# Kernel tuning notes

Hardware: AMD Instinct MI355X
Metric: run time of the kernel (lower is better)

## Reference

```python
import jax, jax.numpy as jnp
import numpy as np

B, S, IN, OUT, H, L, NH, STEPS = 256, 128, 64, 64, 1024, 2, 4, 16
HD = H // NH


def setup_inputs() -> dict:
    key = jax.random.key(0)
    ks = iter(jax.random.split(key, 32))
    std_h = 1.0 / np.sqrt(H)

    def u(k, shape, std):
        return jax.random.uniform(k, shape, jnp.float32, -std, std)

    inp = {"x": jax.random.normal(next(ks), (B, S, IN), jnp.float32)}
    # LSTM cells: stacked gate weights, gate order (i, f, g, o); y = x@Wx + h@Wh + b
    for name, din in (("e0", IN), ("e1", H), ("d0", OUT), ("d1", H)):
        inp[name + "_Wx"] = u(next(ks), (din, 4 * H), std_h)
        inp[name + "_Wh"] = u(next(ks), (H, 4 * H), std_h)
        inp[name + "_b"] = u(next(ks), (4 * H,), std_h)
    # attention linears (x@W + b convention)
    for name in ("Wq", "Wk", "Wv", "Wo"):
        inp[name] = u(next(ks), (H, H), std_h)
    for name in ("bq", "bk", "bv", "bo"):
        inp[name] = u(next(ks), (H,), std_h)
    inp["fc_W"] = u(next(ks), (2 * H, H), 1.0 / np.sqrt(2 * H))
    inp["fc_b"] = u(next(ks), (H,), 1.0 / np.sqrt(2 * H))
    inp["out_W"] = u(next(ks), (H, OUT), std_h)
    inp["out_b"] = u(next(ks), (OUT,), std_h)
    return inp


def _cell(x_t, h, c, Wx, Wh, b):
    z = x_t @ Wx + h @ Wh + b  # [B, 4H]
    i, f, g, o = jnp.split(z, 4, axis=-1)
    c = jax.nn.sigmoid(f) * c + jax.nn.sigmoid(i) * jnp.tanh(g)
    h = jax.nn.sigmoid(o) * jnp.tanh(c)
    return h, c


def _lstm_seq(x, Wx, Wh, b):
    # x: [B, T, D] -> outputs [B, T, H], final (h, c)
    h0 = jnp.zeros((x.shape[0], H), x.dtype)
    def step(carry, xt):
        h, c = carry
        h, c = _cell(xt, h, c, Wx, Wh, b)
        return (h, c), h
    (h, c), ys = jax.lax.scan(step, (h0, h0), jnp.swapaxes(x, 0, 1))
    return jnp.swapaxes(ys, 0, 1), h, c


def reference(x, e0_Wx, e0_Wh, e0_b, e1_Wx, e1_Wh, e1_b,
              d0_Wx, d0_Wh, d0_b, d1_Wx, d1_Wh, d1_b,
              Wq, bq, Wk, bk, Wv, bv, Wo, bo, fc_W, fc_b, out_W, out_b):
    # encoder: 2-layer manual LSTM (dropout=0, eval)
    y0, h0, c0 = _lstm_seq(x, e0_Wx, e0_Wh, e0_b)
    enc_out, h1, c1 = _lstm_seq(y0, e1_Wx, e1_Wh, e1_b)

    # K/V projections of encoder outputs (constant across decoder steps)
    Kp = (enc_out @ Wk + bk).reshape(B, S, NH, HD)
    Vp = (enc_out @ Wv + bv).reshape(B, S, NH, HD)
    scale = float(HD) ** 0.5

    def dstep(carry, _):
        dh0, dc0, dh1, dc1, xin = carry
        dh0, dc0 = _cell(xin, dh0, dc0, d0_Wx, d0_Wh, d0_b)
        dh1, dc1 = _cell(dh0, dh1, dc1, d1_Wx, d1_Wh, d1_b)
        q = (dh1 @ Wq + bq).reshape(B, NH, HD)
        scores = jnp.einsum('bnd,bsnd->bns', q, Kp) / scale
        w = jax.nn.softmax(scores, axis=-1)
        ctx = jnp.einsum('bns,bsnd->bnd', w, Vp).reshape(B, H)
        attn = ctx @ Wo + bo
        comb = jax.nn.relu(jnp.concatenate([dh1, attn], axis=-1) @ fc_W + fc_b)
        out = comb @ out_W + out_b  # [B, OUT]
        return (dh0, dc0, dh1, dc1, out), out

    init = (h0, c0, h1, c1, jnp.zeros((B, OUT), x.dtype))
    _, preds = jax.lax.scan(dstep, init, None, length=STEPS)
    return jnp.swapaxes(preds, 0, 1)  # [B, STEPS, OUT]
```

## Files before the change

kernel.cpp:

```cpp
#include <hip/hip_runtime.h>
#include <math.h>

typedef _Float16 h8 __attribute__((ext_vector_type(8)));
typedef _Float16 h4 __attribute__((ext_vector_type(4)));
typedef float f16v __attribute__((ext_vector_type(16)));

#define HPS 262144
#define XPS 2097152
#define IPS 16384
#define BSTR 40
#define BUFE (128 * BSTR)

__device__ __forceinline__ float4 ld4(const float* p) { return *(const float4*)p; }
__device__ __forceinline__ float sigf(float x) { return 1.0f / (1.0f + expf(-x)); }
__device__ __forceinline__ float bf2f(unsigned short u) { return __uint_as_float(((unsigned)u) << 16); }
__device__ __forceinline__ float rdin(const void* p, size_t i, int bf) {
  return bf ? bf2f(((const unsigned short*)p)[i]) : ((const float*)p)[i];
}

__global__ void detect_dtype(const unsigned short* __restrict__ probe, int n, int* flag) {
  __shared__ int cnt;
  if (threadIdx.x == 0) cnt = 0;
  __syncthreads();
  int c = 0;
  for (int i = threadIdx.x; i < n; i += 256) {
    int e = (probe[i] >> 7) & 0xFF;
    if (e >= 100 && e <= 126) c++;
  }
  atomicAdd(&cnt, c);
  __syncthreads();
  if (threadIdx.x == 0) *flag = (cnt > (n * 3) / 4) ? 1 : 0;
}

__global__ void cvt_f32(const void* __restrict__ in, float* __restrict__ out, int n,
                        const int* __restrict__ flag) {
  int bf = *flag;
  int i = blockIdx.x * 256 + threadIdx.x;
  if (i < n) out[i] = rdin(in, i, bf);
}

__global__ void tsplit(const void* __restrict__ in, int N,
                       _Float16* __restrict__ outHi, _Float16* __restrict__ outLo,
                       int ldo, int kOff, int pOff, const int* __restrict__ flag) {
  __shared__ float tile[32][33];
  int bf = *flag;
  int kb = blockIdx.x * 32, nb = blockIdx.y * 32;
  for (int r = threadIdx.y; r < 32; r += 8)
    tile[threadIdx.x][r] = rdin(in, (size_t)(kb + r) * N + nb + threadIdx.x, bf);
  __syncthreads();
  for (int r = threadIdx.y; r < 32; r += 8) {
    float v = tile[r][threadIdx.x];
    _Float16 hi = (_Float16)v;
    _Float16 lo = (_Float16)(v - (float)hi);
    size_t o = (size_t)(pOff + nb + r) * ldo + kOff + kb + threadIdx.x;
    outHi[o] = hi; outLo[o] = lo;
  }
}

__global__ void f2h_kernel(const void* __restrict__ in, _Float16* __restrict__ out, int n,
                           const int* __restrict__ flag) {
  int bf = *flag;
  int i = blockIdx.x * 1024 + threadIdx.x * 4;
  if (i < n) {
    float vv[4];
#pragma unroll
    for (int k = 0; k < 4; ++k) vv[k] = rdin(in, i + k, bf);
    h4 hv, lv;
#pragma unroll
    for (int k = 0; k < 4; ++k) { hv[k] = (_Float16)vv[k]; lv[k] = (_Float16)(vv[k] - (float)hv[k]); }
    *(h4*)(out + i) = hv;
    *(h4*)(out + n + i) = lv;
  }
}

__global__ void sentinel_kernel(float* out, float v) { out[0] = v; }

__device__ __forceinline__ void gemm_tile(
    const _Float16* __restrict__ A0, int lda0, int aps0,
    const _Float16* __restrict__ A1, int lda1, int aps1, int ksplit,
    const _Float16* __restrict__ WTh, const _Float16* __restrict__ WTl, int ldw,
    int pbase, int c0, int c1,
    float* __restrict__ zp, int zld, _Float16* Bs ) {
  const int tid = threadIdx.x;
  const int wv = tid >> 6, lane = tid & 63;
  const int l31 = lane & 31, lhi = lane >> 5;

  f16v acc00 = {}, acc01 = {}, acc10 = {}, acc11 = {};

  const int r0 = wv * 64 + l31;
  const int r1 = r0 + 32;
  const _Float16* a0b0 = A0 + (size_t)r0 * lda0;
  const _Float16* a1b0 = A1 + (size_t)r0 * lda1;
  const _Float16* a0b1 = A0 + (size_t)r1 * lda0;
  const _Float16* a1b1 = A1 + (size_t)r1 * lda1;

  const int spl = tid >> 7;
  const int sidx = tid & 127;
  const int sp = sidx >> 1;
  const int skh = (sidx & 1) << 4;
  const _Float16* srow = (spl ? WTl : WTh) + (size_t)(pbase + sp) * ldw + skh;
  const int sdoff = (spl * 64 + sp) * BSTR + skh;

  {
    const _Float16* s = srow + (c0 << 5);
    float4 v0 = *(const float4*)(s);
    float4 v1 = *(const float4*)(s + 8);
    _Float16* d = Bs + sdoff;
    *(float4*)(d) = v0;
    *(float4*)(d + 8) = v1;
  }

  int buf = 0;
  for (int c = c0; c < c1; ++c) {
    __syncthreads();
    float4 n0, n1;
    const bool more = (c + 1 < c1);
    if (more) {
      const _Float16* s = srow + ((c + 1) << 5);
      n0 = *(const float4*)(s);
      n1 = *(const float4*)(s + 8);
    }
    const _Float16* bb = Bs + buf * BUFE;
    int k0 = c << 5;
#pragma unroll
    for (int sub = 0; sub < 2; ++sub) {
      int ks = k0 + sub * 16 + lhi * 8;
      const _Float16 *pa0, *pa1; int ap;
      if (ks < ksplit) { pa0 = a0b0 + ks; pa1 = a0b1 + ks; ap = aps0; }
      else { int kk = ks - ksplit; pa0 = a1b0 + kk; pa1 = a1b1 + kk; ap = aps1; }
      h8 af0h = *(const h8*)pa0;
      h8 af0l = *(const h8*)(pa0 + ap);
      h8 af1h = *(const h8*)pa1;
      h8 af1l = *(const h8*)(pa1 + ap);
      int kl = sub * 16 + lhi * 8;
      h8 b0h = *(const h8*)(bb + (size_t)(l31) * BSTR + kl);
      h8 b0l = *(const h8*)(bb + (size_t)(64 + l31) * BSTR + kl);
      h8 b1h = *(const h8*)(bb + (size_t)(32 + l31) * BSTR + kl);
      h8 b1l = *(const h8*)(bb + (size_t)(96 + l31) * BSTR + kl);
      acc00 = __builtin_amdgcn_mfma_f32_32x32x16_f16(af0h, b0h, acc00, 0, 0, 0);
      acc00 = __builtin_amdgcn_mfma_f32_32x32x16_f16(af0h, b0l, acc00, 0, 0, 0);
      acc00 = __builtin_amdgcn_mfma_f32_32x32x16_f16(af0l, b0h, acc00, 0, 0, 0);
      acc01 = __builtin_amdgcn_mfma_f32_32x32x16_f16(af0h, b1h, acc01, 0, 0, 0);
      acc01 = __builtin_amdgcn_mfma_f32_32x32x16_f16(af0h, b1l, acc01, 0, 0, 0);
      acc01 = __builtin_amdgcn_mfma_f32_32x32x16_f16(af0l, b1h, acc01, 0, 0, 0);
      acc10 = __builtin_amdgcn_mfma_f32_32x32x16_f16(af1h, b0h, acc10, 0, 0, 0);
      acc10 = __builtin_amdgcn_mfma_f32_32x32x16_f16(af1h, b0l, acc10, 0, 0, 0);
      acc10 = __builtin_amdgcn_mfma_f32_32x32x16_f16(af1l, b0h, acc10, 0, 0, 0);
      acc11 = __builtin_amdgcn_mfma_f32_32x32x16_f16(af1h, b1h, acc11, 0, 0, 0);
      acc11 = __builtin_amdgcn_mfma_f32_32x32x16_f16(af1h, b1l, acc11, 0, 0, 0);
      acc11 = __builtin_amdgcn_mfma_f32_32x32x16_f16(af1l, b1h, acc11, 0, 0, 0);
    }
    if (more) {
      _Float16* d = Bs + (buf ^ 1) * BUFE + sdoff;
      *(float4*)(d) = n0;
      *(float4*)(d + 8) = n1;
    }
    buf ^= 1;
  }

#pragma unroll
  for (int mi = 0; mi < 2; ++mi) {
#pragma unroll
    for (int ni = 0; ni < 2; ++ni) {
      f16v av = (mi == 0) ? (ni == 0 ? acc00 : acc01) : (ni == 0 ? acc10 : acc11);
      int col = pbase + ni * 32 + l31;
#pragma unroll
      for (int r = 0; r < 16; ++r) {
        int row = wv * 64 + mi * 32 + (r & 3) + ((r >> 2) * 8) + lhi * 4;
        zp[(size_t)row * zld + col] = av[r];
      }
    }
  }
}

__global__ __launch_bounds__(256, 2) void enc_gemm(int t, int l1kq,
    const _Float16* xh, const _Float16* h0, const _Float16* h1,
    const _Float16* wt0h, const _Float16* wt0l,
    const _Float16* wt1h, const _Float16* wt1l,
    const _Float16* wtkvh, const _Float16* wtkvl,
    float* z0, float* z1, float* kvz) {
  __shared__ _Float16 Bs[2 * BUFE];
  int blk = blockIdx.x;
  int nl1 = 64 * l1kq;
  if (blk < nl1) {
    if (t < 1 || t > 128) return;
    int pg = blk & 63, kq = blk >> 6;
    int c0 = (64 * kq) / l1kq, c1 = (64 * (kq + 1)) / l1kq;
    gemm_tile(h0, 1024, HPS, h1, 1024, HPS, 1024, wt1h, wt1l, 2048,
              pg * 64, c0, c1, z1 + (size_t)kq * 1048576, 4096, Bs);
  } else if (blk < nl1 + 128) {
    if (t > 127) return;
    int w = blk - nl1, pg = w & 63, kq = w >> 6;
    gemm_tile(xh + (size_t)t * 64, 8192, XPS, h0, 1024, HPS, 64, wt0h, wt0l, 1088,
              pg * 64, kq * 17, kq * 17 + 17, z0 + (size_t)kq * 1048576, 4096, Bs);
  } else {
    if (t < 2) return;
    int w = blk - nl1 - 128, pg = w & 31, kq = w >> 5;
    gemm_tile(h1, 1024, HPS, h1, 1024, HPS, 1024, wtkvh, wtkvl, 1024,
              pg * 64, kq * 16, kq * 16 + 16, kvz + (size_t)kq * 524288, 2048, Bs);
  }
}

__global__ __launch_bounds__(256, 2) void gemm_k(
    const _Float16* A0, int lda0, int aps0,
    const _Float16* A1, int lda1, int aps1, int ksplit,
    const _Float16* WTh, const _Float16* WTl, int ldw,
    int npg, int nkq, int tot, int kqoff, float* zp, int zld) {
  __shared__ _Float16 Bs[2 * BUFE];
  int pg = blockIdx.x % npg, kq = blockIdx.x / npg + kqoff;
  int c0 = (tot * kq) / nkq, c1 = (tot * (kq + 1)) / nkq;
  gemm_tile(A0, lda0, aps0, A1, lda1, aps1, ksplit, WTh, WTl, ldw,
            pg * 64, c0, c1, zp + (size_t)kq * 256 * zld, zld, Bs);
}

__global__ __launch_bounds__(256, 2) void qfc_kernel(
    const _Float16* h1,
    const _Float16* wqh, const _Float16* wql,
    const _Float16* wfh, const _Float16* wfl,
    float* qp, float* fcp) {
  __shared__ _Float16 Bs[2 * BUFE];
  int blk = blockIdx.x;
  if (blk < 64) {
    int pg = blk & 15, kq = blk >> 4;
    gemm_tile(h1, 1024, HPS, h1, 1024, HPS, 1024, wqh, wql, 1024,
              pg * 64, kq * 8, kq * 8 + 8, qp + (size_t)kq * 262144, 1024, Bs);
  } else {
    int w = blk - 64, pg = w & 15, kq = w >> 4;
    gemm_tile(h1, 1024, HPS, h1, 1024, HPS, 1024, wfh, wfl, 2048,
              pg * 64, kq * 8, kq * 8 + 8, fcp + (size_t)kq * 262144, 1024, Bs);
  }
}

__device__ __forceinline__ void gates_body(const float* __restrict__ zp, int nparts,
    const float* __restrict__ bias, float* __restrict__ c,
    _Float16* __restrict__ h, int blk) {
  int e = blk * 1024 + threadIdx.x * 4;
  int b = e >> 10, j = e & 1023;
  size_t zrow = (size_t)b * 4096;
  float4 vi = ld4(bias + j), vf = ld4(bias + 1024 + j), vg = ld4(bias + 2048 + j), vo = ld4(bias + 3072 + j);
  for (int q = 0; q < nparts; ++q) {
    const float* zq = zp + (size_t)q * 1048576 + zrow;
    float4 t;
    t = ld4(zq + j);        vi.x += t.x; vi.y += t.y; vi.z += t.z; vi.w += t.w;
    t = ld4(zq + 1024 + j); vf.x += t.x; vf.y += t.y; vf.z += t.z; vf.w += t.w;
    t = ld4(zq + 2048 + j); vg.x += t.x; vg.y += t.y; vg.z += t.z; vg.w += t.w;
    t = ld4(zq + 3072 + j); vo.x += t.x; vo.y += t.y; vo.z += t.z; vo.w += t.w;
  }
  float* cp = c + (size_t)b * 1024 + j;
  float4 cv = ld4(cp);
  float zi[4] = {vi.x, vi.y, vi.z, vi.w}, zf[4] = {vf.x, vf.y, vf.z, vf.w};
  float zg[4] = {vg.x, vg.y, vg.z, vg.w}, zo[4] = {vo.x, vo.y, vo.z, vo.w};
  float cc[4] = {cv.x, cv.y, cv.z, cv.w};
  float hn[4];
#pragma unroll
  for (int k = 0; k < 4; ++k) {
    float ii = sigf(zi[k]), ff = sigf(zf[k]), gg = tanhf(zg[k]), oo = sigf(zo[k]);
    float cn = ff * cc[k] + ii * gg;
    cc[k] = cn;
    hn[k] = oo * tanhf(cn);
  }
  float4 co; co.x = cc[0]; co.y = cc[1]; co.z = cc[2]; co.w = cc[3];
  *(float4*)cp = co;
  h4 hv, lv;
#pragma unroll
  for (int k = 0; k < 4; ++k) { hv[k] = (_Float16)hn[k]; lv[k] = (_Float16)(hn[k] - (float)hv[k]); }
  *(h4*)(h + (size_t)b * 1024 + j) = hv;
  *(h4*)(h + HPS + (size_t)b * 1024 + j) = lv;
}

__global__ void enc_gates(int t, int l1parts, const float* z0, const float* z1, const float* kvz,
                          const float* b0, const float* b1,
                          const float* bk, const float* bv,
                          float* c0, float* c1, _Float16* h0, _Float16* h1,
                          _Float16* Kp, _Float16* Vp) {
  int blk = blockIdx.x;
  if (blk < 256) {
    if (t > 127) return;
    gates_body(z0, 2, b0, c0, h0, blk);
  } else if (blk < 512) {
    if (t < 1 || t > 128) return;
    gates_body(z1, l1parts, b1, c1, h1, blk - 256);
  } else {
    if (t < 2) return;
    int e = (blk - 512) * 1024 + threadIdx.x * 4;
    int b = e >> 11, col = e & 2047;
    const float* bb = (col < 1024) ? (bk + col) : (bv + col - 1024);
    float4 v = ld4(bb);
    for (int q = 0; q < 2; ++q) {
      float4 tt = ld4(kvz + (size_t)q * 524288 + e);
      v.x += tt.x; v.y += tt.y; v.z += tt.z; v.w += tt.w;
    }
    _Float16* dst = (col < 1024) ? Kp : Vp;
    int cc = (col < 1024) ? col : col - 1024;
    h4 hv; hv[0] = (_Float16)v.x; hv[1] = (_Float16)v.y; hv[2] = (_Float16)v.z; hv[3] = (_Float16)v.w;
    *(h4*)(dst + (size_t)(b * 128 + (t - 2)) * 1024 + cc) = hv;
  }
}

__global__ void dec_gates(const float* zp, int nparts, const float* bias,
                          float* c, _Float16* h) {
  gates_body(zp, nparts, bias, c, h, blockIdx.x);
}

__global__ void reduce_act(const float* __restrict__ zp, int nparts,
                           const float* __restrict__ bias, _Float16* __restrict__ out, int relu) {
  int e = blockIdx.x * 1024 + threadIdx.x * 4;
  int j = e & 1023;
  float4 v = ld4(bias + j);
  for (int q = 0; q < nparts; ++q) {
    float4 t = ld4(zp + (size_t)q * 262144 + e);
    v.x += t.x; v.y += t.y; v.z += t.z; v.w += t.w;
  }
  if (relu) {
    v.x = fmaxf(v.x, 0.f); v.y = fmaxf(v.y, 0.f); v.z = fmaxf(v.z, 0.f); v.w = fmaxf(v.w, 0.f);
  }
  float vv[4] = {v.x, v.y, v.z, v.w};
  h4 hv, lv;
#pragma unroll
  for (int k = 0; k < 4; ++k) { hv[k] = (_Float16)vv[k]; lv[k] = (_Float16)(vv[k] - (float)hv[k]); }
  *(h4*)(out + e) = hv;
  *(h4*)(out + HPS + e) = lv;
}

__global__ void out_reduce(const float* __restrict__ op, const float* __restrict__ outb,
                           float* __restrict__ dout, _Float16* __restrict__ xin, int s) {
  int e = blockIdx.x * 1024 + threadIdx.x * 4;
  int b = e >> 6, o = e & 63;
  float4 v = ld4(outb + o);
  for (int q = 0; q < 16; ++q) {
    float4 t = ld4(op + (size_t)q * 16384 + e);
    v.x += t.x; v.y += t.y; v.z += t.z; v.w += t.w;
  }
  *(float4*)(dout + (size_t)(b * 16 + s) * 64 + o) = v;
  float vv[4] = {v.x, v.y, v.z, v.w};
  h4 hv, lv;
#pragma unroll
  for (int k = 0; k < 4; ++k) { hv[k] = (_Float16)vv[k]; lv[k] = (_Float16)(vv[k] - (float)hv[k]); }
  *(h4*)(xin + e) = hv;
  *(h4*)(xin + IPS + e) = lv;
}

__global__ void attn_kernel(const float* __restrict__ qp, const float* __restrict__ bq,
                            const _Float16* __restrict__ Kp, const _Float16* __restrict__ Vp,
                            _Float16* __restrict__ ctx) {
  int b = blockIdx.x >> 2, n = blockIdx.x & 3;
  __shared__ float qs[256];
  __shared__ float sw[128];
  int tid = threadIdx.x;
  float qv = bq[n * 256 + tid];
  for (int q = 0; q < 4; ++q) qv += qp[(size_t)q * 262144 + (size_t)b * 1024 + n * 256 + tid];
  qs[tid] = qv;
  __syncthreads();
  int w = tid >> 6, lane = tid & 63;
  for (int s = w; s < 128; s += 4) {
    const _Float16* kr = Kp + (size_t)(b * 128 + s) * 1024 + n * 256;
    float acc = 0.f;
#pragma unroll
    for (int d = 0; d < 4; ++d) acc += qs[lane + d * 64] * (float)kr[lane + d * 64];
    for (int off = 32; off; off >>= 1) acc += __shfl_down(acc, off);
    if (lane == 0) sw[s] = acc * 0.0625f;
  }
  __syncthreads();
  if (w == 0) {
    float a = sw[lane], bb = sw[lane + 64];
    float m = fmaxf(a, bb);
    for (int off = 32; off; off >>= 1) m = fmaxf(m, __shfl_down(m, off));
    m = __shfl(m, 0);
    float e1 = expf(a - m), e2 = expf(bb - m);
    float ss = e1 + e2;
    for (int off = 32; off; off >>= 1) ss += __shfl_down(ss, off);
    ss = __shfl(ss, 0);
    float inv = 1.0f / ss;
    sw[lane] = e1 * inv; sw[lane + 64] = e2 * inv;
  }
  __syncthreads();
  float acc = 0.f;
  const _Float16* vb = Vp + (size_t)b * 131072 + n * 256 + tid;
  for (int s2 = 0; s2 < 128; ++s2) acc += sw[s2] * (float)vb[(size_t)s2 * 1024];
  size_t idx = (size_t)b * 1024 + n * 256 + tid;
  _Float16 hi = (_Float16)acc;
  ctx[idx] = hi;
  ctx[HPS + idx] = (_Float16)(acc - (float)hi);
}

extern "C" void kernel_launch(void* const* d_in, const int* in_sizes, int n_in,
                              void* d_out, int out_size, void* d_ws, size_t ws_size,
                              hipStream_t stream) {
  const void* x     = d_in[0];
  const void* e0_Wx = d_in[1];
  const void* e0_Wh = d_in[2];
  const void* e0_b  = d_in[3];
  const void* e1_Wx = d_in[4];
  const void* e1_Wh = d_in[5];
  const void* e1_b  = d_in[6];
  const void* d0_Wx = d_in[7];
  const void* d0_Wh = d_in[8];
  const void* d0_b  = d_in[9];
  const void* d1_Wx = d_in[10];
  const void* d1_Wh = d_in[11];
  const void* d1_b  = d_in[12];
  const void* Wq = d_in[13];
  const void* Wk = d_in[14];
  const void* Wv = d_in[15];
  const void* Wo = d_in[16];
  const void* bq = d_in[17];
  const void* bk = d_in[18];
  const void* bv = d_in[19];
  const void* bo = d_in[20];
  const void* fc_W  = d_in[21];
  const void* fc_b  = d_in[22];
  const void* out_W = d_in[23];
  const void* out_b = d_in[24];

  int l1parts = 4;
  char* p = (char*)d_ws;
  int* flag; float* bias_arena; char* warena; char* zero0;
  _Float16 *h0, *h1, *xin, *Kp, *Vp, *ctx, *attn_h, *comb;
  float *c0, *c1; float* zarena;
  size_t zeroBytes = 0;

  for (int attempt = 0; attempt < 2; ++attempt) {
    p = (char*)d_ws;
    auto alloc = [&](size_t bytes) { char* r = p; p += (bytes + 255) & ~(size_t)255; return r; };
    flag = (int*)alloc(256);
    bias_arena = (float*)alloc(87040);
    warena = alloc(68419584);
    zero0 = p;
    h0 = (_Float16*)alloc(1048576);
    h1 = (_Float16*)alloc(1048576);
    c0 = (float*)alloc(1048576);
    c1 = (float*)alloc(1048576);
    xin = (_Float16*)alloc(65536);
    zeroBytes = (size_t)(p - zero0);
    Kp = (_Float16*)alloc(67108864);
    Vp = (_Float16*)alloc(67108864);
    zarena = (float*)alloc((size_t)(3 + l1parts) * 4194304);
    ctx    = (_Float16*)alloc(1048576);
    attn_h = (_Float16*)alloc(1048576);
    comb   = (_Float16*)alloc(1048576);
    if ((size_t)(p - (char*)d_ws) <= ws_size) break;
    l1parts = 2;
  }
  if ((size_t)(p - (char*)d_ws) > ws_size) {
    sentinel_kernel<<<1, 1, 0, stream>>>((float*)d_out, 1.0e9f + (float)ws_size);
    return;
  }

  float* c_e0b = bias_arena +     0;
  float* c_e1b = bias_arena +  4096;
  float* c_d0b = bias_arena +  8192;
  float* c_d1b = bias_arena + 12288;
  float* c_bq  = bias_arena + 16384;
  float* c_bk  = bias_arena + 17408;
  float* c_bv  = bias_arena + 18432;
  float* c_bo  = bias_arena + 19456;
  float* c_fcb = bias_arena + 20480;
  float* c_ob  = bias_arena + 21504;

  _Float16* wt_e0h = (_Float16*)(warena);
  _Float16* wt_e0l = (_Float16*)(warena +  8912896);
  _Float16* wt_e1h = (_Float16*)(warena + 17825792);
  _Float16* wt_e1l = (_Float16*)(warena + 34603008);
  _Float16* wt_kvh = (_Float16*)(warena + 51380224);
  _Float16* wt_kvl = (_Float16*)(warena + 55574528);
  _Float16* xh     = (_Float16*)(warena + 59768832);
  _Float16* wt_d0h = (_Float16*)(warena);
  _Float16* wt_d0l = (_Float16*)(warena +  8912896);
  _Float16* wt_d1h = (_Float16*)(warena + 17825792);
  _Float16* wt_d1l = (_Float16*)(warena + 34603008);
  _Float16* wt_qh  = (_Float16*)(warena + 51380224);
  _Float16* wt_ql  = (_Float16*)(warena + 53477376);
  _Float16* wt_oh  = (_Float16*)(warena + 55574528);
  _Float16* wt_ol  = (_Float16*)(warena + 57671680);
  _Float16* wt_fch = (_Float16*)(warena + 59768832);
  _Float16* wt_fcl = (_Float16*)(warena + 63963136);
  _Float16* wt_outh= (_Float16*)(warena + 68157440);
  _Float16* wt_outl= (_Float16*)(warena + 68288512);

  float* z0e = zarena;
  float* z1e = zarena + 2097152;
  float* kvz = z1e + (size_t)l1parts * 1048576;
  float* zdec = zarena;
  float* fcp = zarena;
  float* qp  = zarena + 2097152;
  float* op  = zarena + 3145728;

  detect_dtype<<<1, 256, 0, stream>>>((const unsigned short*)e0_Wx, 16384, flag);
  cvt_f32<<<16, 256, 0, stream>>>(e0_b, c_e0b, 4096, flag);
  cvt_f32<<<16, 256, 0, stream>>>(e1_b, c_e1b, 4096, flag);
  cvt_f32<<<16, 256, 0, stream>>>(d0_b, c_d0b, 4096, flag);
  cvt_f32<<<16, 256, 0, stream>>>(d1_b, c_d1b, 4096, flag);
  cvt_f32<<<4, 256, 0, stream>>>(bq, c_bq, 1024, flag);
  cvt_f32<<<4, 256, 0, stream>>>(bk, c_bk, 1024, flag);
  cvt_f32<<<4, 256, 0, stream>>>(bv, c_bv, 1024, flag);
  cvt_f32<<<4, 256, 0, stream>>>(bo, c_bo, 1024, flag);
  cvt_f32<<<4, 256, 0, stream>>>(fc_b, c_fcb, 1024, flag);
  cvt_f32<<<1, 64, 0, stream>>>(out_b, c_ob, 64, flag);

  dim3 tb(32, 8);
  tsplit<<<dim3(2, 128), tb, 0, stream>>>(e0_Wx, 4096, wt_e0h, wt_e0l, 1088, 0, 0, flag);
  tsplit<<<dim3(32, 128), tb, 0, stream>>>(e0_Wh, 4096, wt_e0h, wt_e0l, 1088, 64, 0, flag);
  tsplit<<<dim3(32, 128), tb, 0, stream>>>(e1_Wx, 4096, wt_e1h, wt_e1l, 2048, 0, 0, flag);
  tsplit<<<dim3(32, 128), tb, 0, stream>>>(e1_Wh, 4096, wt_e1h, wt_e1l, 2048, 1024, 0, flag);
  tsplit<<<dim3(32, 32), tb, 0, stream>>>(Wk, 1024, wt_kvh, wt_kvl, 1024, 0, 0, flag);
  tsplit<<<dim3(32, 32), tb, 0, stream>>>(Wv, 1024, wt_kvh, wt_kvl, 1024, 0, 1024, flag);
  f2h_kernel<<<2048, 256, 0, stream>>>(x, xh, 2097152, flag);
  hipMemsetAsync(zero0, 0, zeroBytes, stream);

  int encBlocks = 64 * l1parts + 192;
  for (int t = 0; t <= 129; ++t) {
    enc_gemm<<<encBlocks, 256, 0, stream>>>(t, l1parts, xh, h0, h1,
                                            wt_e0h, wt_e0l, wt_e1h, wt_e1l,
                                            wt_kvh, wt_kvl, z0e, z1e, kvz);
    enc_gates<<<1024, 256, 0, stream>>>(t, l1parts, z0e, z1e, kvz, c_e0b, c_e1b, c_bk, c_bv,
                                        c0, c1, h0, h1, Kp, Vp);
  }

  tsplit<<<dim3(2, 128), tb, 0, stream>>>(d0_Wx, 4096, wt_d0h, wt_d0l, 1088, 0, 0, flag);
  tsplit<<<dim3(32, 128), tb, 0, stream>>>(d0_Wh, 4096, wt_d0h, wt_d0l, 1088, 64, 0, flag);
  tsplit<<<dim3(32, 128), tb, 0, stream>>>(d1_Wx, 4096, wt_d1h, wt_d1l, 2048, 0, 0, flag);
  tsplit<<<dim3(32, 128), tb, 0, stream>>>(d1_Wh, 4096, wt_d1h, wt_d1l, 2048, 1024, 0, flag);
  tsplit<<<dim3(32, 32), tb, 0, stream>>>(Wq, 1024, wt_qh, wt_ql, 1024, 0, 0, flag);
  tsplit<<<dim3(32, 32), tb, 0, stream>>>(Wo, 1024, wt_oh, wt_ol, 1024, 0, 0, flag);
  tsplit<<<dim3(64, 32), tb, 0, stream>>>(fc_W, 1024, wt_fch, wt_fcl, 2048, 0, 0, flag);
  tsplit<<<dim3(32, 2), tb, 0, stream>>>(out_W, 64, wt_outh, wt_outl, 1024, 0, 0, flag);

  for (int s = 0; s < 16; ++s) {
    gemm_k<<<256, 256, 0, stream>>>(xin, 64, IPS, h0, 1024, HPS, 64,
                                    wt_d0h, wt_d0l, 1088, 64, 4, 34, 0, zdec, 4096);
    dec_gates<<<256, 256, 0, stream>>>(zdec, 4, c_d0b, c0, h0);
    gemm_k<<<256, 256, 0, stream>>>(h0, 1024, HPS, h1, 1024, HPS, 1024,
                                    wt_d1h, wt_d1l, 2048, 64, 4, 64, 0, zdec, 4096);
    dec_gates<<<256, 256, 0, stream>>>(zdec, 4, c_d1b, c1, h1);
    qfc_kernel<<<128, 256, 0, stream>>>(h1, wt_qh, wt_ql, wt_fch, wt_fcl, qp, fcp);
    attn_kernel<<<1024, 256, 0, stream>>>(qp, c_bq, Kp, Vp, ctx);
    gemm_k<<<64, 256, 0, stream>>>(ctx, 1024, HPS, ctx, 1024, HPS, 1024,
                                   wt_oh, wt_ol, 1024, 16, 4, 32, 0, qp, 1024);
    reduce_act<<<256, 256, 0, stream>>>(qp, 4, c_bo, attn_h, 0);
    gemm_k<<<64, 256, 0, stream>>>(h1, 1024, HPS, attn_h, 1024, HPS, 1024,
                                   wt_fch, wt_fcl, 2048, 16, 8, 64, 4, fcp, 1024);
    reduce_act<<<256, 256, 0, stream>>>(fcp, 8, c_fcb, comb, 1);
    gemm_k<<<16, 256, 0, stream>>>(comb, 1024, HPS, comb, 1024, HPS, 1024,
                                   wt_outh, wt_outl, 1024, 1, 16, 32, 0, op, 64);
    out_reduce<<<16, 256, 0, stream>>>(op, c_ob, (float*)d_out, xin, s);
  }
}
```

Baseline: 9.562 ms.

## Fuse split-K reductions and gate activations into GEMM kernels via last-arrival counters

Removes the separate gate, reduce and output-reduction kernels. The last split-K block for each column group now sums the partials and applies the LSTM gates, bias, ReLU or output write, detected through an atomic arrival counter. Gate weight columns are interleaved (i,f,g,o per hidden unit) so one block's 64 columns cover 16 complete hidden units. h buffers are double-buffered to avoid read/write races once finishing happens inside the same launch. This roughly halves the number of kernel launches per recurrence step. In exchange it adds atomics and fences, and the finishing work runs serially in one block per column group.

```diff
diff --git a/kernel.cpp b/kernel.cpp
--- a/kernel.cpp
+++ b/kernel.cpp
@@ -11,6 +11,15 @@
 #define BSTR 40
 #define BUFE (128 * BSTR)
 
+#define COFF_L0 0
+#define COFF_L1 64
+#define COFF_KV 128
+#define COFF_D0 160
+#define COFF_D1 224
+#define COFF_WO 288
+#define COFF_FC 304
+#define COFF_OUT 320
+
 __device__ __forceinline__ float4 ld4(const float* p) { return *(const float4*)p; }
 __device__ __forceinline__ float sigf(float x) { return 1.0f / (1.0f + expf(-x)); }
 __device__ __forceinline__ float bf2f(unsigned short u) { return __uint_as_float(((unsigned)u) << 16); }
@@ -32,16 +41,19 @@
   if (threadIdx.x == 0) *flag = (cnt > (n * 3) / 4) ? 1 : 0;
 }
 
-__global__ void cvt_f32(const void* __restrict__ in, float* __restrict__ out, int n,
+__global__ void cvt_f32(const void* __restrict__ in, float* __restrict__ out, int n, int gp,
                         const int* __restrict__ flag) {
   int bf = *flag;
   int i = blockIdx.x * 256 + threadIdx.x;
-  if (i < n) out[i] = rdin(in, i, bf);
+  if (i < n) {
+    int o = gp ? (((i & 1023) << 2) | (i >> 10)) : i;
+    out[o] = rdin(in, i, bf);
+  }
 }
 
 __global__ void tsplit(const void* __restrict__ in, int N,
                        _Float16* __restrict__ outHi, _Float16* __restrict__ outLo,
-                       int ldo, int kOff, int pOff, const int* __restrict__ flag) {
+                       int ldo, int kOff, int pOff, int gp, const int* __restrict__ flag) {
   __shared__ float tile[32][33];
   int bf = *flag;
   int kb = blockIdx.x * 32, nb = blockIdx.y * 32;
@@ -52,7 +64,9 @@
     float v = tile[r][threadIdx.x];
     _Float16 hi = (_Float16)v;
     _Float16 lo = (_Float16)(v - (float)hi);
-    size_t o = (size_t)(pOff + nb + r) * ldo + kOff + kb + threadIdx.x;
+    int p = pOff + nb + r;
+    if (gp) p = ((p & 1023) << 2) | (p >> 10);
+    size_t o = (size_t)p * ldo + kOff + kb + threadIdx.x;
     outHi[o] = hi; outLo[o] = lo;
   }
 }
@@ -173,171 +187,265 @@
   }
 }
 
+__device__ __forceinline__ bool last_arrival(int* cnt, int nparts) {
+  __shared__ int sdone;
+  __syncthreads();
+  if (threadIdx.x == 0)
+    sdone = __hip_atomic_fetch_add(cnt, 1, __ATOMIC_ACQ_REL, __HIP_MEMORY_SCOPE_AGENT);
+  __syncthreads();
+  if (sdone == nparts - 1) {
+    if (threadIdx.x == 0)
+      __hip_atomic_store(cnt, 0, __ATOMIC_RELAXED, __HIP_MEMORY_SCOPE_AGENT);
+    __threadfence();
+    return true;
+  }
+  return false;
+}
+
+__device__ void lstm_finish(const float* __restrict__ z, size_t ps, int np, int zld,
+                            const float* __restrict__ pb, float* __restrict__ c,
+                            _Float16* __restrict__ h, int pg) {
+  int row = threadIdx.x;
+  const float* zr = z + (size_t)row * zld + pg * 64;
+  float* cr = c + (size_t)row * 1024 + pg * 16;
+  _Float16* hr = h + (size_t)row * 1024 + pg * 16;
+#pragma unroll
+  for (int half = 0; half < 2; ++half) {
+    float4 a[8];
+#pragma unroll
+    for (int u = 0; u < 8; ++u) a[u] = ld4(pb + pg * 64 + half * 32 + u * 4);
+    for (int q = 0; q < np; ++q) {
+      const float* zq = zr + (size_t)q * ps + half * 32;
+#pragma unroll
+      for (int u = 0; u < 8; ++u) {
+        float4 t = ld4(zq + u * 4);
+        a[u].x += t.x; a[u].y += t.y; a[u].z += t.z; a[u].w += t.w;
+      }
+    }
+    float4 cv0 = ld4(cr + half * 8), cv1 = ld4(cr + half * 8 + 4);
+    float cc[8] = {cv0.x, cv0.y, cv0.z, cv0.w, cv1.x, cv1.y, cv1.z, cv1.w};
+    h8 hh, hl;
+#pragma unroll
+    for (int u = 0; u < 8; ++u) {
+      float ii = sigf(a[u].x), ff = sigf(a[u].y), gg = tanhf(a[u].z), oo = sigf(a[u].w);
+      float cn = ff * cc[u] + ii * gg;
+      cc[u] = cn;
+      float hn = oo * tanhf(cn);
+      _Float16 hi = (_Float16)hn;
+      hh[u] = hi; hl[u] = (_Float16)(hn - (float)hi);
+    }
+    float4 co0 = {cc[0], cc[1], cc[2], cc[3]}, co1 = {cc[4], cc[5], cc[6], cc[7]};
+    *(float4*)(cr + half * 8) = co0;
+    *(float4*)(cr + half * 8 + 4) = co1;
+    *(h8*)(hr + half * 8) = hh;
+    *(h8*)(hr + HPS + half * 8) = hl;
+  }
+}
+
+__device__ void kv_finish(const float* __restrict__ z, size_t ps, int np, int zld,
+                          const float* __restrict__ bk, const float* __restrict__ bv,
+                          _Float16* __restrict__ Kp, _Float16* __restrict__ Vp, int pg, int t) {
+  int row = threadIdx.x;
+  int colb = pg * 64;
+  const float* zr = z + (size_t)row * zld + colb;
+  const float* bias = (colb < 1024) ? (bk + colb) : (bv + colb - 1024);
+  _Float16* dst = (colb < 1024) ? (Kp + (size_t)(row * 128 + (t - 2)) * 1024 + colb)
+                                : (Vp + (size_t)(row * 128 + (t - 2)) * 1024 + colb - 1024);
+#pragma unroll
+  for (int u = 0; u < 8; ++u) {
+    float4 a = ld4(bias + u * 8), b = ld4(bias + u * 8 + 4);
+    for (int q = 0; q < np; ++q) {
+      float4 t0 = ld4(zr + (size_t)q * ps + u * 8);
+      float4 t1 = ld4(zr + (size_t)q * ps + u * 8 + 4);
+      a.x += t0.x; a.y += t0.y; a.z += t0.z; a.w += t0.w;
+      b.x += t1.x; b.y += t1.y; b.z += t1.z; b.w += t1.w;
+    }
+    h8 hv;
+    hv[0] = (_Float16)a.x; hv[1] = (_Float16)a.y; hv[2] = (_Float16)a.z; hv[3] = (_Float16)a.w;
+    hv[4] = (_Float16)b.x; hv[5] = (_Float16)b.y; hv[6] = (_Float16)b.z; hv[7] = (_Float16)b.w;
+    *(h8*)(dst + u * 8) = hv;
+  }
+}
+
+__device__ void act_finish(const float* __restrict__ z, size_t ps, int np, int zld,
+                           const float* __restrict__ bias, _Float16* __restrict__ out,
+                           int relu, int pg) {
+  int row = threadIdx.x;
+  const float* zr = z + (size_t)row * zld + pg * 64;
+  _Float16* orow = out + (size_t)row * 1024 + pg * 64;
+#pragma unroll
+  for (int u = 0; u < 8; ++u) {
+    float4 a = ld4(bias + pg * 64 + u * 8), b = ld4(bias + pg * 64 + u * 8 + 4);
+    for (int q = 0; q < np; ++q) {
+      float4 t0 = ld4(zr + (size_t)q * ps + u * 8);
+      float4 t1 = ld4(zr + (size_t)q * ps + u * 8 + 4);
+      a.x += t0.x; a.y += t0.y; a.z += t0.z; a.w += t0.w;
+      b.x += t1.x; b.y += t1.y; b.z += t1.z; b.w += t1.w;
+    }
+    if (relu) {
+      a.x = fmaxf(a.x, 0.f); a.y = fmaxf(a.y, 0.f); a.z = fmaxf(a.z, 0.f); a.w = fmaxf(a.w, 0.f);
+      b.x = fmaxf(b.x, 0.f); b.y = fmaxf(b.y, 0.f); b.z = fmaxf(b.z, 0.f); b.w = fmaxf(b.w, 0.f);
+    }
+    float vv[8] = {a.x, a.y, a.z, a.w, b.x, b.y, b.z, b.w};
+    h8 hh, hl;
+#pragma unroll
+    for (int k = 0; k < 8; ++k) {
+      _Float16 hi = (_Float16)vv[k];
+      hh[k] = hi; hl[k] = (_Float16)(vv[k] - (float)hi);
+    }
+    *(h8*)(orow + u * 8) = hh;
+    *(h8*)(orow + HPS + u * 8) = hl;
+  }
+}
+
+__device__ void out_finish(const float* __restrict__ op, const float* __restrict__ ob,
+                           float* __restrict__ dout, _Float16* __restrict__ xin, int s) {
+  int row = threadIdx.x;
+  const float* zr = op + (size_t)row * 64;
+  float* dr = dout + (size_t)(row * 16 + s) * 64;
+#pragma unroll
+  for (int u = 0; u < 8; ++u) {
+    float4 a = ld4(ob + u * 8), b = ld4(ob + u * 8 + 4);
+    for (int q = 0; q < 16; ++q) {
+      float4 t0 = ld4(zr + (size_t)q * 16384 + u * 8);
+      float4 t1 = ld4(zr + (size_t)q * 16384 + u * 8 + 4);
+      a.x += t0.x; a.y += t0.y; a.z += t0.z; a.w += t0.w;
+      b.x += t1.x; b.y += t1.y; b.z += t1.z; b.w += t1.w;
+    }
+    *(float4*)(dr + u * 8) = a;
+    *(float4*)(dr + u * 8 + 4) = b;
+    float vv[8] = {a.x, a.y, a.z, a.w, b.x, b.y, b.z, b.w};
+    h8 hh, hl;
+#pragma unroll
+    for (int k = 0; k < 8; ++k) {
+      _Float16 hi = (_Float16)vv[k];
+      hh[k] = hi; hl[k] = (_Float16)(vv[k] - (float)hi);
+    }
+    *(h8*)(xin + row * 64 + u * 8) = hh;
+    *(h8*)(xin + IPS + row * 64 + u * 8) = hl;
+  }
+}
+
 __global__ __launch_bounds__(256, 2) void enc_gemm(int t, int l1kq,
-    const _Float16* xh, const _Float16* h0, const _Float16* h1,
+    const _Float16* xh, _Float16* h0a, _Float16* h0b, _Float16* h1a, _Float16* h1b,
     const _Float16* wt0h, const _Float16* wt0l,
     const _Float16* wt1h, const _Float16* wt1l,
     const _Float16* wtkvh, const _Float16* wtkvl,
-    float* z0, float* z1, float* kvz) {
+    float* z0, float* z1, float* kvz,
+    const float* pb0, const float* pb1, const float* bk, const float* bv,
+    float* c0, float* c1, _Float16* Kp, _Float16* Vp, int* cnts) {
   __shared__ _Float16 Bs[2 * BUFE];
   int blk = blockIdx.x;
   int nl1 = 64 * l1kq;
+  const int pr = (t - 1) & 1;
+  const _Float16* h0r = pr ? h0b : h0a;
+  const _Float16* h1r = pr ? h1b : h1a;
   if (blk < nl1) {
     if (t < 1 || t > 128) return;
     int pg = blk & 63, kq = blk >> 6;
-    int c0 = (64 * kq) / l1kq, c1 = (64 * (kq + 1)) / l1kq;
-    gemm_tile(h0, 1024, HPS, h1, 1024, HPS, 1024, wt1h, wt1l, 2048,
-              pg * 64, c0, c1, z1 + (size_t)kq * 1048576, 4096, Bs);
+    int cc0 = (64 * kq) / l1kq, cc1 = (64 * (kq + 1)) / l1kq;
+    gemm_tile(h0r, 1024, HPS, h1r, 1024, HPS, 1024, wt1h, wt1l, 2048,
+              pg * 64, cc0, cc1, z1 + (size_t)kq * 1048576, 4096, Bs);
+    if (last_arrival(cnts + COFF_L1 + pg, l1kq)) {
+      _Float16* h1w = (t & 1) ? h1b : h1a;
+      lstm_finish(z1, 1048576, l1kq, 4096, pb1, c1, h1w, pg);
+    }
   } else if (blk < nl1 + 128) {
     if (t > 127) return;
     int w = blk - nl1, pg = w & 63, kq = w >> 6;
-    gemm_tile(xh + (size_t)t * 64, 8192, XPS, h0, 1024, HPS, 64, wt0h, wt0l, 1088,
+    gemm_tile(xh + (size_t)t * 64, 8192, XPS, h0r, 1024, HPS, 64, wt0h, wt0l, 1088,
               pg * 64, kq * 17, kq * 17 + 17, z0 + (size_t)kq * 1048576, 4096, Bs);
+    if (last_arrival(cnts + COFF_L0 + pg, 2)) {
+      _Float16* h0w = (t & 1) ? h0b : h0a;
+      lstm_finish(z0, 1048576, 2, 4096, pb0, c0, h0w, pg);
+    }
   } else {
     if (t < 2) return;
     int w = blk - nl1 - 128, pg = w & 31, kq = w >> 5;
-    gemm_tile(h1, 1024, HPS, h1, 1024, HPS, 1024, wtkvh, wtkvl, 1024,
+    gemm_tile(h1r, 1024, HPS, h1r, 1024, HPS, 1024, wtkvh, wtkvl, 1024,
               pg * 64, kq * 16, kq * 16 + 16, kvz + (size_t)kq * 524288, 2048, Bs);
-  }
-}
-
-__global__ __launch_bounds__(256, 2) void gemm_k(
-    const _Float16* A0, int lda0, int aps0,
-    const _Float16* A1, int lda1, int aps1, int ksplit,
-    const _Float16* WTh, const _Float16* WTl, int ldw,
-    int npg, int nkq, int tot, int kqoff, float* zp, int zld) {
+    if (last_arrival(cnts + COFF_KV + pg, 2)) {
+      kv_finish(kvz, 524288, 2, 2048, bk, bv, Kp, Vp, pg, t);
+    }
+  }
+}
+
+__global__ __launch_bounds__(256, 2) void dec0_gemm(
+    const _Float16* xin, const _Float16* h0r,
+    const _Float16* wh, const _Float16* wl, const float* pb,
+    float* c0, _Float16* h0w, float* z, int* cnt) {
   __shared__ _Float16 Bs[2 * BUFE];
-  int pg = blockIdx.x % npg, kq = blockIdx.x / npg + kqoff;
-  int c0 = (tot * kq) / nkq, c1 = (tot * (kq + 1)) / nkq;
-  gemm_tile(A0, lda0, aps0, A1, lda1, aps1, ksplit, WTh, WTl, ldw,
-            pg * 64, c0, c1, zp + (size_t)kq * 256 * zld, zld, Bs);
+  int pg = blockIdx.x & 63, kq = blockIdx.x >> 6;
+  int cc0 = (34 * kq) / 4, cc1 = (34 * (kq + 1)) / 4;
+  gemm_tile(xin, 64, IPS, h0r, 1024, HPS, 64, wh, wl, 1088,
+            pg * 64, cc0, cc1, z + (size_t)kq * 1048576, 4096, Bs);
+  if (last_arrival(cnt + pg, 4))
+    lstm_finish(z, 1048576, 4, 4096, pb, c0, h0w, pg);
+}
+
+__global__ __launch_bounds__(256, 2) void dec1_gemm(
+    const _Float16* h0n, const _Float16* h1r,
+    const _Float16* wh, const _Float16* wl, const float* pb,
+    float* c1, _Float16* h1w, float* z, int* cnt) {
+  __shared__ _Float16 Bs[2 * BUFE];
+  int pg = blockIdx.x & 63, kq = blockIdx.x >> 6;
+  gemm_tile(h0n, 1024, HPS, h1r, 1024, HPS, 1024, wh, wl, 2048,
+            pg * 64, kq * 16, kq * 16 + 16, z + (size_t)kq * 1048576, 4096, Bs);
+  if (last_arrival(cnt + pg, 4))
+    lstm_finish(z, 1048576, 4, 4096, pb, c1, h1w, pg);
 }
 
 __global__ __launch_bounds__(256, 2) void qfc_kernel(
-    const _Float16* h1,
+    const _Float16* h1n,
     const _Float16* wqh, const _Float16* wql,
     const _Float16* wfh, const _Float16* wfl,
-    float* qp, float* fcp) {
+    float* qp, float* fcp, int* cnt_fc) {
   __shared__ _Float16 Bs[2 * BUFE];
   int blk = blockIdx.x;
   if (blk < 64) {
     int pg = blk & 15, kq = blk >> 4;
-    gemm_tile(h1, 1024, HPS, h1, 1024, HPS, 1024, wqh, wql, 1024,
+    gemm_tile(h1n, 1024, HPS, h1n, 1024, HPS, 1024, wqh, wql, 1024,
               pg * 64, kq * 8, kq * 8 + 8, qp + (size_t)kq * 262144, 1024, Bs);
   } else {
     int w = blk - 64, pg = w & 15, kq = w >> 4;
-    gemm_tile(h1, 1024, HPS, h1, 1024, HPS, 1024, wfh, wfl, 2048,
+    gemm_tile(h1n, 1024, HPS, h1n, 1024, HPS, 1024, wfh, wfl, 2048,
               pg * 64, kq * 8, kq * 8 + 8, fcp + (size_t)kq * 262144, 1024, Bs);
-  }
-}
-
-__device__ __forceinline__ void gates_body(const float* __restrict__ zp, int nparts,
-    const float* __restrict__ bias, float* __restrict__ c,
-    _Float16* __restrict__ h, int blk) {
-  int e = blk * 1024 + threadIdx.x * 4;
-  int b = e >> 10, j = e & 1023;
-  size_t zrow = (size_t)b * 4096;
-  float4 vi = ld4(bias + j), vf = ld4(bias + 1024 + j), vg = ld4(bias + 2048 + j), vo = ld4(bias + 3072 + j);
-  for (int q = 0; q < nparts; ++q) {
-    const float* zq = zp + (size_t)q * 1048576 + zrow;
-    float4 t;
-    t = ld4(zq + j);        vi.x += t.x; vi.y += t.y; vi.z += t.z; vi.w += t.w;
-    t = ld4(zq + 1024 + j); vf.x += t.x; vf.y += t.y; vf.z += t.z; vf.w += t.w;
-    t = ld4(zq + 2048 + j); vg.x += t.x; vg.y += t.y; vg.z += t.z; vg.w += t.w;
-    t = ld4(zq + 3072 + j); vo.x += t.x; vo.y += t.y; vo.z += t.z; vo.w += t.w;
-  }
-  float* cp = c + (size_t)b * 1024 + j;
-  float4 cv = ld4(cp);
-  float zi[4] = {vi.x, vi.y, vi.z, vi.w}, zf[4] = {vf.x, vf.y, vf.z, vf.w};
-  float zg[4] = {vg.x, vg.y, vg.z, vg.w}, zo[4] = {vo.x, vo.y, vo.z, vo.w};
-  float cc[4] = {cv.x, cv.y, cv.z, cv.w};
-  float hn[4];
-#pragma unroll
-  for (int k = 0; k < 4; ++k) {
-    float ii = sigf(zi[k]), ff = sigf(zf[k]), gg = tanhf(zg[k]), oo = sigf(zo[k]);
-    float cn = ff * cc[k] + ii * gg;
-    cc[k] = cn;
-    hn[k] = oo * tanhf(cn);
-  }
-  float4 co; co.x = cc[0]; co.y = cc[1]; co.z = cc[2]; co.w = cc[3];
-  *(float4*)cp = co;
-  h4 hv, lv;
-#pragma unroll
-  for (int k = 0; k < 4; ++k) { hv[k] = (_Float16)hn[k]; lv[k] = (_Float16)(hn[k] - (float)hv[k]); }
-  *(h4*)(h + (size_t)b * 1024 + j) = hv;
-  *(h4*)(h + HPS + (size_t)b * 1024 + j) = lv;
-}
-
-__global__ void enc_gates(int t, int l1parts, const float* z0, const float* z1, const float* kvz,
-                          const float* b0, const float* b1,
-                          const float* bk, const float* bv,
-                          float* c0, float* c1, _Float16* h0, _Float16* h1,
-                          _Float16* Kp, _Float16* Vp) {
-  int blk = blockIdx.x;
-  if (blk < 256) {
-    if (t > 127) return;
-    gates_body(z0, 2, b0, c0, h0, blk);
-  } else if (blk < 512) {
-    if (t < 1 || t > 128) return;
-    gates_body(z1, l1parts, b1, c1, h1, blk - 256);
-  } else {
-    if (t < 2) return;
-    int e = (blk - 512) * 1024 + threadIdx.x * 4;
-    int b = e >> 11, col = e & 2047;
-    const float* bb = (col < 1024) ? (bk + col) : (bv + col - 1024);
-    float4 v = ld4(bb);
-    for (int q = 0; q < 2; ++q) {
-      float4 tt = ld4(kvz + (size_t)q * 524288 + e);
-      v.x += tt.x; v.y += tt.y; v.z += tt.z; v.w += tt.w;
-    }
-    _Float16* dst = (col < 1024) ? Kp : Vp;
-    int cc = (col < 1024) ? col : col - 1024;
-    h4 hv; hv[0] = (_Float16)v.x; hv[1] = (_Float16)v.y; hv[2] = (_Float16)v.z; hv[3] = (_Float16)v.w;
-    *(h4*)(dst + (size_t)(b * 128 + (t - 2)) * 1024 + cc) = hv;
-  }
-}
-
-__global__ void dec_gates(const float* zp, int nparts, const float* bias,
-                          float* c, _Float16* h) {
-  gates_body(zp, nparts, bias, c, h, blockIdx.x);
-}
-
-__global__ void reduce_act(const float* __restrict__ zp, int nparts,
-                           const float* __restrict__ bias, _Float16* __restrict__ out, int relu) {
-  int e = blockIdx.x * 1024 + threadIdx.x * 4;
-  int j = e & 1023;
-  float4 v = ld4(bias + j);
-  for (int q = 0; q < nparts; ++q) {
-    float4 t = ld4(zp + (size_t)q * 262144 + e);
-    v.x += t.x; v.y += t.y; v.z += t.z; v.w += t.w;
-  }
-  if (relu) {
-    v.x = fmaxf(v.x, 0.f); v.y = fmaxf(v.y, 0.f); v.z = fmaxf(v.z, 0.f); v.w = fmaxf(v.w, 0.f);
-  }
-  float vv[4] = {v.x, v.y, v.z, v.w};
-  h4 hv, lv;
-#pragma unroll
-  for (int k = 0; k < 4; ++k) { hv[k] = (_Float16)vv[k]; lv[k] = (_Float16)(vv[k] - (float)hv[k]); }
-  *(h4*)(out + e) = hv;
-  *(h4*)(out + HPS + e) = lv;
-}
-
-__global__ void out_reduce(const float* __restrict__ op, const float* __restrict__ outb,
-                           float* __restrict__ dout, _Float16* __restrict__ xin, int s) {
-  int e = blockIdx.x * 1024 + threadIdx.x * 4;
-  int b = e >> 6, o = e & 63;
-  float4 v = ld4(outb + o);
-  for (int q = 0; q < 16; ++q) {
-    float4 t = ld4(op + (size_t)q * 16384 + e);
-    v.x += t.x; v.y += t.y; v.z += t.z; v.w += t.w;
-  }
-  *(float4*)(dout + (size_t)(b * 16 + s) * 64 + o) = v;
-  float vv[4] = {v.x, v.y, v.z, v.w};
-  h4 hv, lv;
-#pragma unroll
-  for (int k = 0; k < 4; ++k) { hv[k] = (_Float16)vv[k]; lv[k] = (_Float16)(vv[k] - (float)hv[k]); }
-  *(h4*)(xin + e) = hv;
-  *(h4*)(xin + IPS + e) = lv;
+    last_arrival(cnt_fc + pg, 8);
+  }
+}
+
+__global__ __launch_bounds__(256, 2) void wo_gemm(
+    const _Float16* ctx, const _Float16* wh, const _Float16* wl,
+    const float* bo, _Float16* attn_h, float* z, int* cnt) {
+  __shared__ _Float16 Bs[2 * BUFE];
+  int pg = blockIdx.x & 15, kq = blockIdx.x >> 4;
+  gemm_tile(ctx, 1024, HPS, ctx, 1024, HPS, 1024, wh, wl, 1024,
+            pg * 64, kq * 8, kq * 8 + 8, z + (size_t)kq * 262144, 1024, Bs);
+  if (last_arrival(cnt + pg, 4))
+    act_finish(z, 262144, 4, 1024, bo, attn_h, 0, pg);
+}
+
+__global__ __launch_bounds__(256, 2) void fc_gemm(
+    const _Float16* h1n, const _Float16* attn_h,
+    const _Float16* wh, const _Float16* wl,
+    const float* fcb, _Float16* comb, float* z, int* cnt) {
+  __shared__ _Float16 Bs[2 * BUFE];
+  int pg = blockIdx.x & 15, kq = (blockIdx.x >> 4) + 4;
+  gemm_tile(h1n, 1024, HPS, attn_h, 1024, HPS, 1024, wh, wl, 2048,
+            pg * 64, kq * 8, kq * 8 + 8, z + (size_t)kq * 262144, 1024, Bs);
+  if (last_arrival(cnt + pg, 8))
+    act_finish(z, 262144, 8, 1024, fcb, comb, 1, pg);
+}
+
+__global__ __launch_bounds__(256, 2) void out_gemm(
+    const _Float16* comb, const _Float16* wh, const _Float16* wl,
+    const float* ob, float* dout, _Float16* xin, float* z, int s, int* cnt) {
+  __shared__ _Float16 Bs[2 * BUFE];
+  int kq = blockIdx.x;
+  gemm_tile(comb, 1024, HPS, comb, 1024, HPS, 1024, wh, wl, 1024,
+            0, kq * 2, kq * 2 + 2, z + (size_t)kq * 16384, 64, Bs);
+  if (last_arrival(cnt, 16))
+    out_finish(z, ob, dout, xin, s);
 }
 
 __global__ void attn_kernel(const float* __restrict__ qp, const float* __restrict__ bq,
@@ -415,7 +523,8 @@
   int l1parts = 4;
   char* p = (char*)d_ws;
   int* flag; float* bias_arena; char* warena; char* zero0;
-  _Float16 *h0, *h1, *xin, *Kp, *Vp, *ctx, *attn_h, *comb;
+  int* cnts;
+  _Float16 *h0a, *h0b, *h1a, *h1b, *xin, *Kp, *Vp, *ctx, *attn_h, *comb;
   float *c0, *c1; float* zarena;
   size_t zeroBytes = 0;
 
@@ -426,8 +535,11 @@
     bias_arena = (float*)alloc(87040);
     warena = alloc(68419584);
     zero0 = p;
-    h0 = (_Float16*)alloc(1048576);
-    h1 = (_Float16*)alloc(1048576);
+    cnts = (int*)alloc(2048);
+    h0a = (_Float16*)alloc(1048576);
+    h0b = (_Float16*)alloc(1048576);
+    h1a = (_Float16*)alloc(1048576);
+    h1b = (_Float16*)alloc(1048576);
     c0 = (float*)alloc(1048576);
     c1 = (float*)alloc(1048576);
     xin = (_Float16*)alloc(65536);
@@ -486,62 +598,61 @@
   float* op  = zarena + 3145728;
 
   detect_dtype<<<1, 256, 0, stream>>>((const unsigned short*)e0_Wx, 16384, flag);
-  cvt_f32<<<16, 256, 0, stream>>>(e0_b, c_e0b, 4096, flag);
-  cvt_f32<<<16, 256, 0, stream>>>(e1_b, c_e1b, 4096, flag);
-  cvt_f32<<<16, 256, 0, stream>>>(d0_b, c_d0b, 4096, flag);
-  cvt_f32<<<16, 256, 0, stream>>>(d1_b, c_d1b, 4096, flag);
-  cvt_f32<<<4, 256, 0, stream>>>(bq, c_bq, 1024, flag);
-  cvt_f32<<<4, 256, 0, stream>>>(bk, c_bk, 1024, flag);
-  cvt_f32<<<4, 256, 0, stream>>>(bv, c_bv, 1024, flag);
-  cvt_f32<<<4, 256, 0, stream>>>(bo, c_bo, 1024, flag);
-  cvt_f32<<<4, 256, 0, stream>>>(fc_b, c_fcb, 1024, flag);
-  cvt_f32<<<1, 64, 0, stream>>>(out_b, c_ob, 64, flag);
+  cvt_f32<<<16, 256, 0, stream>>>(e0_b, c_e0b, 4096, 1, flag);
+  cvt_f32<<<16, 256, 0, stream>>>(e1_b, c_e1b, 4096, 1, flag);
+  cvt_f32<<<16, 256, 0, stream>>>(d0_b, c_d0b, 4096, 1, flag);
+  cvt_f32<<<16, 256, 0, stream>>>(d1_b, c_d1b, 4096, 1, flag);
+  cvt_f32<<<4, 256, 0, stream>>>(bq, c_bq, 1024, 0, flag);
+  cvt_f32<<<4, 256, 0, stream>>>(bk, c_bk, 1024, 0, flag);
+  cvt_f32<<<4, 256, 0, stream>>>(bv, c_bv, 1024, 0, flag);
+  cvt_f32<<<4, 256, 0, stream>>>(bo, c_bo, 1024, 0, flag);
+  cvt_f32<<<4, 256, 0, stream>>>(fc_b, c_fcb, 1024, 0, flag);
+  cvt_f32<<<1, 64, 0, stream>>>(out_b, c_ob, 64, 0, flag);
 
   dim3 tb(32, 8);
-  tsplit<<<dim3(2, 128), tb, 0, stream>>>(e0_Wx, 4096, wt_e0h, wt_e0l, 1088, 0, 0, flag);
-  tsplit<<<dim3(32, 128), tb, 0, stream>>>(e0_Wh, 4096, wt_e0h, wt_e0l, 1088, 64, 0, flag);
-  tsplit<<<dim3(32, 128), tb, 0, stream>>>(e1_Wx, 4096, wt_e1h, wt_e1l, 2048, 0, 0, flag);
-  tsplit<<<dim3(32, 128), tb, 0, stream>>>(e1_Wh, 4096, wt_e1h, wt_e1l, 2048, 1024, 0, flag);
-  tsplit<<<dim3(32, 32), tb, 0, stream>>>(Wk, 1024, wt_kvh, wt_kvl, 1024, 0, 0, flag);
-  tsplit<<<dim3(32, 32), tb, 0, stream>>>(Wv, 1024, wt_kvh, wt_kvl, 1024, 0, 1024, flag);
+  tsplit<<<dim3(2, 128), tb, 0, stream>>>(e0_Wx, 4096, wt_e0h, wt_e0l, 1088, 0, 0, 1, flag);
+  tsplit<<<dim3(32, 128), tb, 0, stream>>>(e0_Wh, 4096, wt_e0h, wt_e0l, 1088, 64, 0, 1, flag);
+  tsplit<<<dim3(32, 128), tb, 0, stream>>>(e1_Wx, 4096, wt_e1h, wt_e1l, 2048, 0, 0, 1, flag);
+  tsplit<<<dim3(32, 128), tb, 0, stream>>>(e1_Wh, 4096, wt_e1h, wt_e1l, 2048, 1024, 0, 1, flag);
+  tsplit<<<dim3(32, 32), tb, 0, stream>>>(Wk, 1024, wt_kvh, wt_kvl, 1024, 0, 0, 0, flag);
+  tsplit<<<dim3(32, 32), tb, 0, stream>>>(Wv, 1024, wt_kvh, wt_kvl, 1024, 0, 1024, 0, flag);
   f2h_kernel<<<2048, 256, 0, stream>>>(x, xh, 2097152, flag);
   hipMemsetAsync(zero0, 0, zeroBytes, stream);
 
   int encBlocks = 64 * l1parts + 192;
   for (int t = 0; t <= 129; ++t) {
-    enc_gemm<<<encBlocks, 256, 0, stream>>>(t, l1parts, xh, h0, h1,
+    enc_gemm<<<encBlocks, 256, 0, stream>>>(t, l1parts, xh, h0a, h0b, h1a, h1b,
                                             wt_e0h, wt_e0l, wt_e1h, wt_e1l,
-                                            wt_kvh, wt_kvl, z0e, z1e, kvz);
-    enc_gates<<<1024, 256, 0, stream>>>(t, l1parts, z0e, z1e, kvz, c_e0b, c_e1b, c_bk, c_bv,
-                                        c0, c1, h0, h1, Kp, Vp);
-  }
-
-  tsplit<<<dim3(2, 128), tb, 0, stream>>>(d0_Wx, 4096, wt_d0h, wt_d0l, 1088, 0, 0, flag);
-  tsplit<<<dim3(32, 128), tb, 0, stream>>>(d0_Wh, 4096, wt_d0h, wt_d0l, 1088, 64, 0, flag);
-  tsplit<<<dim3(32, 128), tb, 0, stream>>>(d1_Wx, 4096, wt_d1h, wt_d1l, 2048, 0, 0, flag);
-  tsplit<<<dim3(32, 128), tb, 0, stream>>>(d1_Wh, 4096, wt_d1h, wt_d1l, 2048, 1024, 0, flag);
-  tsplit<<<dim3(32, 32), tb, 0, stream>>>(Wq, 1024, wt_qh, wt_ql, 1024, 0, 0, flag);
-  tsplit<<<dim3(32, 32), tb, 0, stream>>>(Wo, 1024, wt_oh, wt_ol, 1024, 0, 0, flag);
-  tsplit<<<dim3(64, 32), tb, 0, stream>>>(fc_W, 1024, wt_fch, wt_fcl, 2048, 0, 0, flag);
-  tsplit<<<dim3(32, 2), tb, 0, stream>>>(out_W, 64, wt_outh, wt_outl, 1024, 0, 0, flag);
+                                            wt_kvh, wt_kvl, z0e, z1e, kvz,
+                                            c_e0b, c_e1b, c_bk, c_bv,
+                                            c0, c1, Kp, Vp, cnts);
+  }
+
+  tsplit<<<dim3(2, 128), tb, 0, stream>>>(d0_Wx, 4096, wt_d0h, wt_d0l, 1088, 0, 0, 1, flag);
+  tsplit<<<dim3(32, 128), tb, 0, stream>>>(d0_Wh, 4096, wt_d0h, wt_d0l, 1088, 64, 0, 1, flag);
+  tsplit<<<dim3(32, 128), tb, 0, stream>>>(d1_Wx, 4096, wt_d1h, wt_d1l, 2048, 0, 0, 1, flag);
+  tsplit<<<dim3(32, 128), tb, 0, stream>>>(d1_Wh, 4096, wt_d1h, wt_d1l, 2048, 1024, 0, 1, flag);
+  tsplit<<<dim3(32, 32), tb, 0, stream>>>(Wq, 1024, wt_qh, wt_ql, 1024, 0, 0, 0, flag);
+  tsplit<<<dim3(32, 32), tb, 0, stream>>>(Wo, 1024, wt_oh, wt_ol, 1024, 0, 0, 0, flag);
+  tsplit<<<dim3(64, 32), tb, 0, stream>>>(fc_W, 1024, wt_fch, wt_fcl, 2048, 0, 0, 0, flag);
+  tsplit<<<dim3(32, 2), tb, 0, stream>>>(out_W, 64, wt_outh, wt_outl, 1024, 0, 0, 0, flag);
 
   for (int s = 0; s < 16; ++s) {
-    gemm_k<<<256, 256, 0, stream>>>(xin, 64, IPS, h0, 1024, HPS, 64,
-                                    wt_d0h, wt_d0l, 1088, 64, 4, 34, 0, zdec, 4096);
-    dec_gates<<<256, 256, 0, stream>>>(zdec, 4, c_d0b, c0, h0);
-    gemm_k<<<256, 256, 0, stream>>>(h0, 1024, HPS, h1, 1024, HPS, 1024,
-                                    wt_d1h, wt_d1l, 2048, 64, 4, 64, 0, zdec, 4096);
-    dec_gates<<<256, 256, 0, stream>>>(zdec, 4, c_d1b, c1, h1);
-    qfc_kernel<<<128, 256, 0, stream>>>(h1, wt_qh, wt_ql, wt_fch, wt_fcl, qp, fcp);
+    const _Float16* h0r = (s & 1) ? h0a : h0b;
+    _Float16* h0w = (s & 1) ? h0b : h0a;
+    const _Float16* h1r = (s & 1) ? h1b : h1a;
+    _Float16* h1w = (s & 1) ? h1a : h1b;
+    dec0_gemm<<<256, 256, 0, stream>>>(xin, h0r, wt_d0h, wt_d0l, c_d0b, c0, h0w,
+                                       zdec, cnts + COFF_D0);
+    dec1_gemm<<<256, 256, 0, stream>>>(h0w, h1r, wt_d1h, wt_d1l, c_d1b, c1, h1w,
+                                       zdec, cnts + COFF_D1);
+    qfc_kernel<<<128, 256, 0, stream>>>(h1w, wt_qh, wt_ql, wt_fch, wt_fcl, qp, fcp,
+                                        cnts + COFF_FC);
     attn_kernel<<<1024, 256, 0, stream>>>(qp, c_bq, Kp, Vp, ctx);
-    gemm_k<<<64, 256, 0, stream>>>(ctx, 1024, HPS, ctx, 1024, HPS, 1024,
-                                   wt_oh, wt_ol, 1024, 16, 4, 32, 0, qp, 1024);
-    reduce_act<<<256, 256, 0, stream>>>(qp, 4, c_bo, attn_h, 0);
-    gemm_k<<<64, 256, 0, stream>>>(h1, 1024, HPS, attn_h, 1024, HPS, 1024,
-                                   wt_fch, wt_fcl, 2048, 16, 8, 64, 4, fcp, 1024);
-    reduce_act<<<256, 256, 0, stream>>>(fcp, 8, c_fcb, comb, 1);
-    gemm_k<<<16, 256, 0, stream>>>(comb, 1024, HPS, comb, 1024, HPS, 1024,
-                                   wt_outh, wt_outl, 1024, 1, 16, 32, 0, op, 64);
-    out_reduce<<<16, 256, 0, stream>>>(op, c_ob, (float*)d_out, xin, s);
-  }
-}
+    wo_gemm<<<64, 256, 0, stream>>>(ctx, wt_oh, wt_ol, c_bo, attn_h, qp, cnts + COFF_WO);
+    fc_gemm<<<64, 256, 0, stream>>>(h1w, attn_h, wt_fch, wt_fcl, c_fcb, comb, fcp,
+                                    cnts + COFF_FC);
+    out_gemm<<<16, 256, 0, stream>>>(comb, wt_outh, wt_outl, c_ob, (float*)d_out, xin,
+                                     op, s, cnts + COFF_OUT);
+  }
+}
```

Measured after the change: 17.63 ms. 84.4% more time.
